# Optimization experiments

Measured on AMD Instinct MI355X. Metric: run time of the kernel, lower is better.

Reference implementation:

```python
import jax, jax.numpy as jnp
import numpy as np

IN_CH = 256
BOT = IN_CH // 2  # bottleneck channels
B, W, H = 4, 64, 64


def setup_inputs() -> dict:
    key = jax.random.key(0)
    ks = jax.random.split(key, 10)
    s_in = 1.0 / np.sqrt(IN_CH)   # torch Conv2d default init scale (kaiming-ish bound)
    s_bt = 1.0 / np.sqrt(BOT)
    return {
        "X": jax.random.normal(ks[0], (B, IN_CH, W, H), dtype=jnp.float32),
        "Wq": jax.random.uniform(ks[1], (BOT, IN_CH), jnp.float32, -s_in, s_in),
        "bq": jax.random.uniform(ks[2], (BOT,), jnp.float32, -s_in, s_in),
        "Wk": jax.random.uniform(ks[3], (BOT, IN_CH), jnp.float32, -s_in, s_in),
        "bk": jax.random.uniform(ks[4], (BOT,), jnp.float32, -s_in, s_in),
        "Wv": jax.random.uniform(ks[5], (BOT, IN_CH), jnp.float32, -s_in, s_in),
        "bv": jax.random.uniform(ks[6], (BOT,), jnp.float32, -s_in, s_in),
        "Wo": jax.random.uniform(ks[7], (IN_CH, BOT), jnp.float32, -s_bt, s_bt),
        "bo": jax.random.uniform(ks[8], (IN_CH,), jnp.float32, -s_bt, s_bt),
        "gamma": 0.1 * jax.random.normal(ks[9], (1,), dtype=jnp.float32),
    }


def reference(X, Wq, bq, Wk, bk, Wv, bv, Wo, bo, gamma):
    b, c, w, h = X.shape
    n = w * h
    Xf = X.reshape(b, c, n)  # [b, c, n] — 1x1 conv == per-pixel linear
    q = jnp.einsum('oc,bcn->bon', Wq, Xf) + bq[None, :, None]  # [b, c/2, n]
    k = jnp.einsum('oc,bcn->bon', Wk, Xf) + bk[None, :, None]
    v = jnp.einsum('oc,bcn->bon', Wv, Xf) + bv[None, :, None]
    # score[b,i,j] = sum_c q[b,c,i] * k[b,c,j]; softmax over dim=1 (query index i)
    score = jnp.einsum('bci,bcj->bij', q, k)          # [b, n, n]
    attn = jax.nn.softmax(score, axis=1)
    out = jnp.einsum('bci,bij->bcj', v, attn)         # [b, c/2, n]
    out = jnp.einsum('oc,bcn->bon', Wo, out) + bo[None, :, None]  # [b, c, n]
    out = out.reshape(b, c, w, h)
    return gamma[0] * out + X
```

## Files before the change

kernel.cpp:

```cpp
#include <hip/hip_runtime.h>
#include <math.h>

#define NBATCH 4
#define CIN    256
#define CBOT   128
#define NPIX   4096
#define NPART  4
#define LOG2E  1.44269504f

typedef __attribute__((ext_vector_type(4))) float f32x4;
typedef __attribute__((ext_vector_type(8))) short bf16x8;

__device__ __forceinline__ unsigned short f2bf(float f) {
    union { float f; unsigned u; } v; v.f = f;
    unsigned r = (v.u + 0x7FFFu + ((v.u >> 16) & 1u)) >> 16;
    return (unsigned short)r;
}
__device__ __forceinline__ unsigned pk2bf(float a, float b) {
#if __has_builtin(__builtin_amdgcn_cvt_pk_bf16_f32)
    auto r = __builtin_amdgcn_cvt_pk_bf16_f32(a, b);
    unsigned u; __builtin_memcpy(&u, &r, 4); return u;
#else
    unsigned r;
    asm("v_cvt_pk_bf16_f32 %0, %1, %2" : "=v"(r) : "v"(a), "v"(b));
    return r;
#endif
}
__device__ __forceinline__ float fexp2(float x) {
#if __has_builtin(__builtin_amdgcn_exp2f)
    return __builtin_amdgcn_exp2f(x);
#else
    float r;
    asm("v_exp_f32 %0, %1" : "=v"(r) : "v"(x));
    return r;
#endif
}
__device__ __forceinline__ void plswap32(unsigned &a, unsigned &b) {
#if __has_builtin(__builtin_amdgcn_permlane32_swap)
    auto r = __builtin_amdgcn_permlane32_swap(a, b, false, false);
    a = (unsigned)r[0]; b = (unsigned)r[1];
#else
    asm volatile("v_permlane32_swap_b32 %0, %1" : "+v"(a), "+v"(b));
#endif
}
__device__ __forceinline__ void plswap16(unsigned &a, unsigned &b) {
#if __has_builtin(__builtin_amdgcn_permlane16_swap)
    auto r = __builtin_amdgcn_permlane16_swap(a, b, false, false);
    a = (unsigned)r[0]; b = (unsigned)r[1];
#else
    asm volatile("v_permlane16_swap_b32 %0, %1" : "+v"(a), "+v"(b));
#endif
}

__global__ __launch_bounds__(256) void k_wcvt(
    const float* __restrict__ Wq, const float* __restrict__ Wk,
    const float* __restrict__ Wv, const float* __restrict__ Wo,
    unsigned short* __restrict__ Wb)
{
    const int f4 = (blockIdx.x * 256 + threadIdx.x) * 4;
    const int reg = f4 >> 15, loc = f4 & 32767;
    const float* __restrict__ W = (reg == 0) ? Wq : (reg == 1) ? Wk : (reg == 2) ? Wv : Wo;
    const float sc = (reg == 1) ? LOG2E : 1.f;
    float4 v = *(const float4*)(W + loc);
    uint2 u;
    u.x = pk2bf(v.x * sc, v.y * sc);
    u.y = pk2bf(v.z * sc, v.w * sc);
    *(uint2*)&Wb[f4] = u;
}

__global__ __launch_bounds__(256) void k_qkvx(
    const float* __restrict__ X,
    const unsigned short* __restrict__ Wb,
    const float* __restrict__ bq, const float* __restrict__ bk,
    const float* __restrict__ bv,
    unsigned short* __restrict__ Qt, unsigned short* __restrict__ Kt,
    unsigned short* __restrict__ Vt)
{
    __shared__ __align__(16) unsigned short Xs[32][264];
    const int tid = threadIdx.x;
    const int wv = tid >> 6, lane = tid & 63;
    const int grp = lane & 15, quad = lane >> 4;
    const int pbase = blockIdx.x * 32;
    const int b     = blockIdx.y;
    const float* __restrict__ Xg = X + (size_t)b * CIN * NPIX + pbase;

#pragma unroll
    for (int k = 0; k < 8; ++k) {
        int f = tid + 256 * k;
        int c = f >> 3, pg = (f & 7) << 2;
        float4 v = *(const float4*)(Xg + (size_t)c * NPIX + pg);
        unsigned uxy = pk2bf(v.x, v.y);
        unsigned uzw = pk2bf(v.z, v.w);
        Xs[pg + 0][c] = (unsigned short)uxy;
        Xs[pg + 1][c] = (unsigned short)(uxy >> 16);
        Xs[pg + 2][c] = (unsigned short)uzw;
        Xs[pg + 3][c] = (unsigned short)(uzw >> 16);
    }
    __syncthreads();

    const unsigned short* __restrict__ Wqb = Wb;
    const unsigned short* __restrict__ Wkb = Wb + 32768;
    const unsigned short* __restrict__ Wvb = Wb + 65536;
    const int obase = 32 * wv;

    f32x4 aQ[2][2], aK[2][2], aV[2][2];
#pragma unroll
    for (int mt = 0; mt < 2; ++mt)
#pragma unroll
        for (int nt = 0; nt < 2; ++nt) {
            aQ[mt][nt] = (f32x4)0.f; aK[mt][nt] = (f32x4)0.f; aV[mt][nt] = (f32x4)0.f;
        }

    for (int ks = 0; ks < 8; ++ks) {
        bf16x8 bx[2];
#pragma unroll
        for (int nt = 0; nt < 2; ++nt)
            bx[nt] = *(const bf16x8*)&Xs[nt * 16 + grp][ks * 32 + quad * 8];
        bf16x8 wq_[2], wk_[2], wv_[2];
#pragma unroll
        for (int mt = 0; mt < 2; ++mt) {
            const size_t roff = (size_t)(obase + mt * 16 + grp) * CIN + ks * 32 + quad * 8;
            wq_[mt] = *(const bf16x8*)&Wqb[roff];
            wk_[mt] = *(const bf16x8*)&Wkb[roff];
            wv_[mt] = *(const bf16x8*)&Wvb[roff];
        }
#pragma unroll
        for (int mt = 0; mt < 2; ++mt)
#pragma unroll
            for (int nt = 0; nt < 2; ++nt) {
                aQ[mt][nt] = __builtin_amdgcn_mfma_f32_16x16x32_bf16(wq_[mt], bx[nt], aQ[mt][nt], 0, 0, 0);
                aK[mt][nt] = __builtin_amdgcn_mfma_f32_16x16x32_bf16(wk_[mt], bx[nt], aK[mt][nt], 0, 0, 0);
                aV[mt][nt] = __builtin_amdgcn_mfma_f32_16x16x32_bf16(bx[mt], wv_[nt], aV[mt][nt], 0, 0, 0);
            }
    }

    unsigned short* Qb_ = Qt + (size_t)b * NPIX * CBOT;
    unsigned short* Kb_ = Kt + (size_t)b * NPIX * CBOT;
#pragma unroll
    for (int mt = 0; mt < 2; ++mt) {
        int o0 = obase + mt * 16 + quad * 4;
        float b4q[4], b4k[4];
#pragma unroll
        for (int r = 0; r < 4; ++r) { b4q[r] = bq[o0 + r]; b4k[r] = bk[o0 + r] * LOG2E; }
#pragma unroll
        for (int nt = 0; nt < 2; ++nt) {
            int p = pbase + nt * 16 + grp;
            uint2 uq, uk;
            uq.x = pk2bf(aQ[mt][nt][0] + b4q[0], aQ[mt][nt][1] + b4q[1]);
            uq.y = pk2bf(aQ[mt][nt][2] + b4q[2], aQ[mt][nt][3] + b4q[3]);
            uk.x = pk2bf(aK[mt][nt][0] + b4k[0], aK[mt][nt][1] + b4k[1]);
            uk.y = pk2bf(aK[mt][nt][2] + b4k[2], aK[mt][nt][3] + b4k[3]);
            *(uint2*)&Qb_[(size_t)p * CBOT + o0] = uq;
            *(uint2*)&Kb_[(size_t)p * CBOT + o0] = uk;
        }
    }
    unsigned short* Vb_ = Vt + (size_t)b * CBOT * NPIX;
#pragma unroll
    for (int nt = 0; nt < 2; ++nt) {
        int o = obase + nt * 16 + grp;
        float bb = bv[o];
#pragma unroll
        for (int mt = 0; mt < 2; ++mt) {
            int p0 = pbase + mt * 16 + quad * 4;
            uint2 u;
            u.x = pk2bf(aV[mt][nt][0] + bb, aV[mt][nt][1] + bb);
            u.y = pk2bf(aV[mt][nt][2] + bb, aV[mt][nt][3] + bb);
            *(uint2*)&Vb_[(size_t)o * NPIX + p0] = u;
        }
    }
}

__global__ __launch_bounds__(256, 2) void k_flash(
    const unsigned short* __restrict__ Qt,
    const unsigned short* __restrict__ Kt,
    const unsigned short* __restrict__ Vt,
    unsigned short* __restrict__ Opart,
    float* __restrict__ Lpart)
{
    extern __shared__ __align__(16) unsigned short lds[];
#define QS(bi, r, c) lds[(bi) * 8704 + (r) * 136 + (c)]
#define VS(bi, r, c) lds[17408 + (bi) * 9216 + (r) * 72 + (c)]
    const int tid  = threadIdx.x;
    const int wv   = tid >> 6, lane = tid & 63;
    const int grp  = lane & 15, quad = lane >> 4;
    const int jblk = blockIdx.x * 128;
    const int part = blockIdx.y;
    const int b    = blockIdx.z;
    const int tbeg = part * (64 / NPART);
    const int tend = tbeg + (64 / NPART);
    const unsigned short* __restrict__ Qb = Qt + (size_t)b * NPIX * CBOT;
    const unsigned short* __restrict__ Kb = Kt + (size_t)b * NPIX * CBOT;
    const unsigned short* __restrict__ Vb = Vt + (size_t)b * CBOT * NPIX;

    bf16x8 bk[2][4];
#pragma unroll
    for (int nt = 0; nt < 2; ++nt)
#pragma unroll
        for (int ks = 0; ks < 4; ++ks)
            bk[nt][ks] = *(const bf16x8*)&Kb[
                (size_t)(jblk + wv * 32 + nt * 16 + grp) * CBOT + ks * 32 + quad * 8];

    bf16x8 aones;
#pragma unroll
    for (int t = 0; t < 8; ++t) aones[t] = (short)0x3F80;

    f32x4 o[8][2];
#pragma unroll
    for (int ct = 0; ct < 8; ++ct) { o[ct][0] = (f32x4)0.f; o[ct][1] = (f32x4)0.f; }
    f32x4 lacc[2] = {(f32x4)0.f, (f32x4)0.f};

    const int qrow = tid >> 4, qch = tid & 15;
    const int vrow = tid >> 3, vch = tid & 7;
    bf16x8 qreg[4], vreg[4];
#pragma unroll
    for (int k = 0; k < 4; ++k) {
        qreg[k] = *(const bf16x8*)&Qb[(size_t)(tbeg * 64 + qrow + 16 * k) * CBOT + qch * 8];
        vreg[k] = *(const bf16x8*)&Vb[(size_t)(vrow + 32 * k) * NPIX + tbeg * 64 + vch * 8];
    }
#pragma unroll
    for (int k = 0; k < 4; ++k) {
        *(bf16x8*)&QS(0, qrow + 16 * k, qch * 8) = qreg[k];
        *(bf16x8*)&VS(0, vrow + 32 * k, vch * 8) = vreg[k];
    }
    {
        const int i1 = (tbeg + 1) * 64;
#pragma unroll
        for (int k = 0; k < 4; ++k) {
            qreg[k] = *(const bf16x8*)&Qb[(size_t)(i1 + qrow + 16 * k) * CBOT + qch * 8];
            vreg[k] = *(const bf16x8*)&Vb[(size_t)(vrow + 32 * k) * NPIX + i1 + vch * 8];
        }
    }
    __syncthreads();

    for (int it = tbeg; it < tend; ++it) {
        const int cur = (it - tbeg) & 1;

        f32x4 sf[4][2];
#pragma unroll
        for (int mt = 0; mt < 4; ++mt) { sf[mt][0] = (f32x4)0.f; sf[mt][1] = (f32x4)0.f; }
        __builtin_amdgcn_s_setprio(1);
#pragma unroll
        for (int mt = 0; mt < 4; ++mt)
#pragma unroll
            for (int ks = 0; ks < 4; ++ks) {
                bf16x8 aq_ = *(const bf16x8*)&QS(cur, mt * 16 + grp, ks * 32 + quad * 8);
                sf[mt][0] = __builtin_amdgcn_mfma_f32_16x16x32_bf16(aq_, bk[0][ks], sf[mt][0], 0, 0, 0);
                sf[mt][1] = __builtin_amdgcn_mfma_f32_16x16x32_bf16(aq_, bk[1][ks], sf[mt][1], 0, 0, 0);
            }
        __builtin_amdgcn_s_setprio(0);

        if (it + 1 < tend) {
#pragma unroll
            for (int k = 0; k < 4; ++k) {
                *(bf16x8*)&QS(cur ^ 1, qrow + 16 * k, qch * 8) = qreg[k];
                *(bf16x8*)&VS(cur ^ 1, vrow + 32 * k, vch * 8) = vreg[k];
            }
            if (it + 2 < tend) {
                const int i2 = (it + 2) * 64;
#pragma unroll
                for (int k = 0; k < 4; ++k) {
                    qreg[k] = *(const bf16x8*)&Qb[(size_t)(i2 + qrow + 16 * k) * CBOT + qch * 8];
                    vreg[k] = *(const bf16x8*)&Vb[(size_t)(vrow + 32 * k) * NPIX + i2 + vch * 8];
                }
            }
        }

        bf16x8 pf[2][2];
#pragma unroll
        for (int nt = 0; nt < 2; ++nt)
#pragma unroll
            for (int h = 0; h < 2; ++h) {
                unsigned u0a = pk2bf(fexp2(sf[2 * h][nt][0]),     fexp2(sf[2 * h][nt][1]));
                unsigned u1a = pk2bf(fexp2(sf[2 * h][nt][2]),     fexp2(sf[2 * h][nt][3]));
                unsigned u0b = pk2bf(fexp2(sf[2 * h + 1][nt][0]), fexp2(sf[2 * h + 1][nt][1]));
                unsigned u1b = pk2bf(fexp2(sf[2 * h + 1][nt][2]), fexp2(sf[2 * h + 1][nt][3]));
                plswap32(u0a, u0b); plswap16(u0a, u0b);
                plswap32(u1a, u1b); plswap16(u1a, u1b);
                union { unsigned u[4]; bf16x8 v; } cvt;
                cvt.u[0] = u0a; cvt.u[1] = u1a; cvt.u[2] = u0b; cvt.u[3] = u1b;
                pf[nt][h] = cvt.v;
            }

        __builtin_amdgcn_s_setprio(1);
#pragma unroll
        for (int ct = 0; ct < 8; ++ct)
#pragma unroll
            for (int h = 0; h < 2; ++h) {
                bf16x8 av_ = *(const bf16x8*)&VS(cur, ct * 16 + grp, h * 32 + quad * 8);
                o[ct][0] = __builtin_amdgcn_mfma_f32_16x16x32_bf16(av_, pf[0][h], o[ct][0], 0, 0, 0);
                o[ct][1] = __builtin_amdgcn_mfma_f32_16x16x32_bf16(av_, pf[1][h], o[ct][1], 0, 0, 0);
            }
#pragma unroll
        for (int nt = 0; nt < 2; ++nt) {
            lacc[nt] = __builtin_amdgcn_mfma_f32_16x16x32_bf16(aones, pf[nt][0], lacc[nt], 0, 0, 0);
            lacc[nt] = __builtin_amdgcn_mfma_f32_16x16x32_bf16(aones, pf[nt][1], lacc[nt], 0, 0, 0);
        }
        __builtin_amdgcn_s_setprio(0);

        if (it + 1 < tend) __syncthreads();
    }

    unsigned short* Ob = Opart + ((size_t)(part * NBATCH + b) * NPIX + jblk) * CBOT;
#pragma unroll
    for (int nt = 0; nt < 2; ++nt) {
        const size_t jrow = (size_t)(wv * 32 + nt * 16 + grp) * CBOT;
#pragma unroll
        for (int ct = 0; ct < 8; ++ct) {
            uint2 u;
            u.x = pk2bf(o[ct][nt][0], o[ct][nt][1]);
            u.y = pk2bf(o[ct][nt][2], o[ct][nt][3]);
            *(uint2*)&Ob[jrow + ct * 16 + quad * 4] = u;
        }
    }
    if (quad == 0) {
#pragma unroll
        for (int nt = 0; nt < 2; ++nt)
            Lpart[(size_t)(part * NBATCH + b) * NPIX + jblk + wv * 32 + nt * 16 + grp] =
                lacc[nt][0];
    }
#undef QS
#undef VS
}

__global__ __launch_bounds__(256) void k_oproj(
    const unsigned short* __restrict__ Opart, const float* __restrict__ Lpart,
    const unsigned short* __restrict__ Wob, const float* __restrict__ bo,
    const float* __restrict__ gamma, const float* __restrict__ X,
    float* __restrict__ Out)
{
    const int tid = threadIdx.x;
    const int wv = tid >> 6, lane = tid & 63;
    const int grp = lane & 15, quad = lane >> 4;
    const int pbase = blockIdx.x * 32;
    const int b     = blockIdx.y;
    const int obase = 64 * wv;

    f32x4 acc[2][4];
#pragma unroll
    for (int mt = 0; mt < 2; ++mt)
#pragma unroll
        for (int nt = 0; nt < 4; ++nt) acc[mt][nt] = (f32x4)0.f;

    for (int ks = 0; ks < 4; ++ks) {
        bf16x8 bw[4];
#pragma unroll
        for (int nt = 0; nt < 4; ++nt)
            bw[nt] = *(const bf16x8*)&Wob[(size_t)(obase + nt * 16 + grp) * CBOT + ks * 32 + quad * 8];
#pragma unroll
        for (int mt = 0; mt < 2; ++mt) {
            int p = pbase + mt * 16 + grp;
#pragma unroll
            for (int part = 0; part < NPART; ++part) {
                bf16x8 ao = *(const bf16x8*)&Opart[
                    ((size_t)(part * NBATCH + b) * NPIX + p) * CBOT + ks * 32 + quad * 8];
#pragma unroll
                for (int nt = 0; nt < 4; ++nt)
                    acc[mt][nt] = __builtin_amdgcn_mfma_f32_16x16x32_bf16(ao, bw[nt], acc[mt][nt], 0, 0, 0);
            }
        }
    }

    float linv[2][4];
#pragma unroll
    for (int mt = 0; mt < 2; ++mt)
#pragma unroll
        for (int r = 0; r < 4; ++r) {
            int p = pbase + mt * 16 + quad * 4 + r;
            float ls = 0.f;
#pragma unroll
            for (int part = 0; part < NPART; ++part)
                ls += Lpart[(size_t)(part * NBATCH + b) * NPIX + p];
            linv[mt][r] = 1.f / ls;
        }
    float g = gamma[0];
#pragma unroll
    for (int nt = 0; nt < 4; ++nt) {
        int o = obase + nt * 16 + grp;
        float bb = bo[o];
#pragma unroll
        for (int mt = 0; mt < 2; ++mt) {
            int p0 = pbase + mt * 16 + quad * 4;
            size_t base = (size_t)b * CIN * NPIX + (size_t)o * NPIX + p0;
            float4 x4 = *(const float4*)(X + base);
            float4 r4;
            r4.x = g * (acc[mt][nt][0] * linv[mt][0] + bb) + x4.x;
            r4.y = g * (acc[mt][nt][1] * linv[mt][1] + bb) + x4.y;
            r4.z = g * (acc[mt][nt][2] * linv[mt][2] + bb) + x4.z;
            r4.w = g * (acc[mt][nt][3] * linv[mt][3] + bb) + x4.w;
            *(float4*)(Out + base) = r4;
        }
    }
}

extern "C" void kernel_launch(void* const* d_in, const int* in_sizes, int n_in,
                              void* d_out, int out_size, void* d_ws, size_t ws_size,
                              hipStream_t stream)
{
    (void)in_sizes; (void)n_in; (void)out_size; (void)ws_size;
    const float* X     = (const float*)d_in[0];
    const float* Wq    = (const float*)d_in[1];
    const float* bq    = (const float*)d_in[2];
    const float* Wk    = (const float*)d_in[3];
    const float* bk    = (const float*)d_in[4];
    const float* Wv    = (const float*)d_in[5];
    const float* bv    = (const float*)d_in[6];
    const float* Wo    = (const float*)d_in[7];
    const float* bo    = (const float*)d_in[8];
    const float* gamma = (const float*)d_in[9];
    float* out = (float*)d_out;

    const size_t BNC = (size_t)NBATCH * NPIX * CBOT;
    unsigned short* Qt    = (unsigned short*)d_ws;
    unsigned short* Kt    = Qt + BNC;
    unsigned short* Vt    = Kt + BNC;
    unsigned short* Opart = Vt + BNC;
    float*          Lpart = (float*)(Opart + (size_t)NPART * BNC);
    unsigned short* Wb    = (unsigned short*)(Lpart + (size_t)NPART * NBATCH * NPIX);

    const int flash_lds = 2 * (64 * 136 + 128 * 72) * 2;

    k_wcvt <<<dim3(128),               256, 0,         stream>>>(Wq, Wk, Wv, Wo, Wb);
    k_qkvx <<<dim3(128, NBATCH),       256, 0,         stream>>>(X, Wb, bq, bk, bv, Qt, Kt, Vt);
    k_flash<<<dim3(32, NPART, NBATCH), 256, flash_lds, stream>>>(Qt, Kt, Vt, Opart, Lpart);
    k_oproj<<<dim3(128, NBATCH),       256, 0,         stream>>>(Opart, Lpart, Wb + 98304, bo, gamma, X, out);
}
```

Measured before the change: 158.4 us.

## Single-buffer flash LDS, double the query partitions, raise occupancy, remap blocks

```diff
diff --git a/kernel.cpp b/kernel.cpp
--- a/kernel.cpp
+++ b/kernel.cpp
@@ -5,7 +5,7 @@
 #define CIN    256
 #define CBOT   128
 #define NPIX   4096
-#define NPART  4
+#define NPART  8
 #define LOG2E  1.44269504f
 
 typedef __attribute__((ext_vector_type(4))) float f32x4;
@@ -170,22 +170,27 @@
     }
 }
 
-__global__ __launch_bounds__(256, 2) void k_flash(
+__global__ __launch_bounds__(256, 4) void k_flash(
     const unsigned short* __restrict__ Qt,
     const unsigned short* __restrict__ Kt,
     const unsigned short* __restrict__ Vt,
     unsigned short* __restrict__ Opart,
     float* __restrict__ Lpart)
 {
-    extern __shared__ __align__(16) unsigned short lds[];
-#define QS(bi, r, c) lds[(bi) * 8704 + (r) * 136 + (c)]
-#define VS(bi, r, c) lds[17408 + (bi) * 9216 + (r) * 72 + (c)]
+    __shared__ __align__(16) unsigned short Qs[64][136];
+    __shared__ __align__(16) unsigned short Vs[128][72];
     const int tid  = threadIdx.x;
     const int wv   = tid >> 6, lane = tid & 63;
     const int grp  = lane & 15, quad = lane >> 4;
-    const int jblk = blockIdx.x * 128;
-    const int part = blockIdx.y;
-    const int b    = blockIdx.z;
+
+    const int x    = blockIdx.x;
+    const int y    = blockIdx.y;
+    const int z    = blockIdx.z;
+    const int pbN  = (x & 7) * 4 + z;
+    const int jp   = (x >> 3) + 4 * y;
+    const int part = pbN & 7;
+    const int b    = pbN >> 3;
+    const int jblk = jp * 128;
     const int tbeg = part * (64 / NPART);
     const int tend = tbeg + (64 / NPART);
     const unsigned short* __restrict__ Qb = Qt + (size_t)b * NPIX * CBOT;
@@ -219,8 +224,8 @@
     }
 #pragma unroll
     for (int k = 0; k < 4; ++k) {
-        *(bf16x8*)&QS(0, qrow + 16 * k, qch * 8) = qreg[k];
-        *(bf16x8*)&VS(0, vrow + 32 * k, vch * 8) = vreg[k];
+        *(bf16x8*)&Qs[qrow + 16 * k][qch * 8] = qreg[k];
+        *(bf16x8*)&Vs[vrow + 32 * k][vch * 8] = vreg[k];
     }
     {
         const int i1 = (tbeg + 1) * 64;
@@ -233,8 +238,6 @@
     __syncthreads();
 
     for (int it = tbeg; it < tend; ++it) {
-        const int cur = (it - tbeg) & 1;
-
         f32x4 sf[4][2];
 #pragma unroll
         for (int mt = 0; mt < 4; ++mt) { sf[mt][0] = (f32x4)0.f; sf[mt][1] = (f32x4)0.f; }
@@ -243,27 +246,11 @@
         for (int mt = 0; mt < 4; ++mt)
 #pragma unroll
             for (int ks = 0; ks < 4; ++ks) {
-                bf16x8 aq_ = *(const bf16x8*)&QS(cur, mt * 16 + grp, ks * 32 + quad * 8);
+                bf16x8 aq_ = *(const bf16x8*)&Qs[mt * 16 + grp][ks * 32 + quad * 8];
                 sf[mt][0] = __builtin_amdgcn_mfma_f32_16x16x32_bf16(aq_, bk[0][ks], sf[mt][0], 0, 0, 0);
                 sf[mt][1] = __builtin_amdgcn_mfma_f32_16x16x32_bf16(aq_, bk[1][ks], sf[mt][1], 0, 0, 0);
             }
         __builtin_amdgcn_s_setprio(0);
-
-        if (it + 1 < tend) {
-#pragma unroll
-            for (int k = 0; k < 4; ++k) {
-                *(bf16x8*)&QS(cur ^ 1, qrow + 16 * k, qch * 8) = qreg[k];
-                *(bf16x8*)&VS(cur ^ 1, vrow + 32 * k, vch * 8) = vreg[k];
-            }
-            if (it + 2 < tend) {
-                const int i2 = (it + 2) * 64;
-#pragma unroll
-                for (int k = 0; k < 4; ++k) {
-                    qreg[k] = *(const bf16x8*)&Qb[(size_t)(i2 + qrow + 16 * k) * CBOT + qch * 8];
-                    vreg[k] = *(const bf16x8*)&Vb[(size_t)(vrow + 32 * k) * NPIX + i2 + vch * 8];
-                }
-            }
-        }
 
         bf16x8 pf[2][2];
 #pragma unroll
@@ -286,7 +273,7 @@
         for (int ct = 0; ct < 8; ++ct)
 #pragma unroll
             for (int h = 0; h < 2; ++h) {
-                bf16x8 av_ = *(const bf16x8*)&VS(cur, ct * 16 + grp, h * 32 + quad * 8);
+                bf16x8 av_ = *(const bf16x8*)&Vs[ct * 16 + grp][h * 32 + quad * 8];
                 o[ct][0] = __builtin_amdgcn_mfma_f32_16x16x32_bf16(av_, pf[0][h], o[ct][0], 0, 0, 0);
                 o[ct][1] = __builtin_amdgcn_mfma_f32_16x16x32_bf16(av_, pf[1][h], o[ct][1], 0, 0, 0);
             }
@@ -297,10 +284,27 @@
         }
         __builtin_amdgcn_s_setprio(0);
 
-        if (it + 1 < tend) __syncthreads();
-    }
-
-    unsigned short* Ob = Opart + ((size_t)(part * NBATCH + b) * NPIX + jblk) * CBOT;
+        if (it + 1 < tend) {
+            __syncthreads();
+#pragma unroll
+            for (int k = 0; k < 4; ++k) {
+                *(bf16x8*)&Qs[qrow + 16 * k][qch * 8] = qreg[k];
+                *(bf16x8*)&Vs[vrow + 32 * k][vch * 8] = vreg[k];
+            }
+            if (it + 2 < tend) {
+                const int i2 = (it + 2) * 64;
+#pragma unroll
+                for (int k = 0; k < 4; ++k) {
+                    qreg[k] = *(const bf16x8*)&Qb[(size_t)(i2 + qrow + 16 * k) * CBOT + qch * 8];
+                    vreg[k] = *(const bf16x8*)&Vb[(size_t)(vrow + 32 * k) * NPIX + i2 + vch * 8];
+                }
+            }
+            __syncthreads();
+        }
+    }
+
+    const int pbI = part * NBATCH + b;
+    unsigned short* Ob = Opart + ((size_t)pbI * NPIX + jblk) * CBOT;
 #pragma unroll
     for (int nt = 0; nt < 2; ++nt) {
         const size_t jrow = (size_t)(wv * 32 + nt * 16 + grp) * CBOT;
@@ -315,11 +319,9 @@
     if (quad == 0) {
 #pragma unroll
         for (int nt = 0; nt < 2; ++nt)
-            Lpart[(size_t)(part * NBATCH + b) * NPIX + jblk + wv * 32 + nt * 16 + grp] =
+            Lpart[(size_t)pbI * NPIX + jblk + wv * 32 + nt * 16 + grp] =
                 lacc[nt][0];
     }
-#undef QS
-#undef VS
 }
 
 __global__ __launch_bounds__(256) void k_oproj(
@@ -417,10 +419,8 @@
     float*          Lpart = (float*)(Opart + (size_t)NPART * BNC);
     unsigned short* Wb    = (unsigned short*)(Lpart + (size_t)NPART * NBATCH * NPIX);
 
-    const int flash_lds = 2 * (64 * 136 + 128 * 72) * 2;
-
-    k_wcvt <<<dim3(128),               256, 0,         stream>>>(Wq, Wk, Wv, Wo, Wb);
-    k_qkvx <<<dim3(128, NBATCH),       256, 0,         stream>>>(X, Wb, bq, bk, bv, Qt, Kt, Vt);
-    k_flash<<<dim3(32, NPART, NBATCH), 256, flash_lds, stream>>>(Qt, Kt, Vt, Opart, Lpart);
-    k_oproj<<<dim3(128, NBATCH),       256, 0,         stream>>>(Opart, Lpart, Wb + 98304, bo, gamma, X, out);
-}
+    k_wcvt <<<dim3(128),               256, 0, stream>>>(Wq, Wk, Wv, Wo, Wb);
+    k_qkvx <<<dim3(128, NBATCH),       256, 0, stream>>>(X, Wb, bq, bk, bv, Qt, Kt, Vt);
+    k_flash<<<dim3(32, NPART, NBATCH), 256, 0, stream>>>(Qt, Kt, Vt, Opart, Lpart);
+    k_oproj<<<dim3(128, NBATCH),       256, 0, stream>>>(Opart, Lpart, Wb + 98304, bo, gamma, X, out);
+}
```

After: 272.5 us. 1.72x slower.
